# Optimization experiments

Measured on AMD Instinct MI355X. Metric: run time of the kernel, lower is better.

Reference implementation:

```python
import jax, jax.numpy as jnp
import numpy as np

D = 1024      # d_model
H = 16        # n_heads
KVH = 4       # num_kv_heads
DH = D // H   # head_dim = 64
CHUNK = 256
SDIM = 128
MG = 8        # m_global
B, T = 4, 4096


def setup_inputs() -> dict:
    key = jax.random.key(0)
    ks = jax.random.split(key, 12)
    s = 0.02
    mk = lambda i, shape: jax.random.normal(ks[i], shape, jnp.float32) * s
    return dict(
        x=jax.random.normal(ks[0], (B, T, D), jnp.float32),
        state=jnp.zeros((B, SDIM), jnp.float32),
        Wq=mk(1, (D, D)), Wk=mk(2, (KVH * DH, D)), Wv=mk(3, (KVH * DH, D)),
        Wo=mk(4, (D, D)), bo=jnp.zeros((D,), jnp.float32),
        ln_attn_g=jnp.ones((D,), jnp.float32), ln_attn_b=jnp.zeros((D,), jnp.float32),
        ln_ffn_g=jnp.ones((D,), jnp.float32), ln_ffn_b=jnp.zeros((D,), jnp.float32),
        W1=mk(5, (4 * D, D)), b1=jnp.zeros((4 * D,), jnp.float32),
        W2=mk(6, (D, 4 * D)), b2=jnp.zeros((D,), jnp.float32),
        Wsp=mk(7, (SDIM, D)), bsp=jnp.zeros((SDIM,), jnp.float32),
        Wsi=mk(8, (D, SDIM)), bsi=jnp.zeros((D,), jnp.float32),
        gtok=mk(9, (MG, D)),
    )


def _ln(x, g, b):
    m = x.mean(-1, keepdims=True)
    v = ((x - m) ** 2).mean(-1, keepdims=True)
    return (x - m) / jnp.sqrt(v + 1e-5) * g + b


def reference(x, state, Wq, Wk, Wv, Wo, bo, ln_attn_g, ln_attn_b,
              ln_ffn_g, ln_ffn_b, W1, b1, W2, b2, Wsp, bsp, Wsi, bsi, gtok):
    Bn, Tn, Dn = x.shape
    nchunks = Tn // CHUNK
    Tc = MG + CHUNK            # tokens per attention call (globals + chunk)
    G = H // KVH               # query heads per KV head
    causal = jnp.tril(jnp.ones((Tc, Tc), bool))
    scale = 1.0 / np.sqrt(DH).astype(np.float32)

    def step(st, chunk):  # st:[B,SDIM], chunk:[B,CHUNK,D]
        h = _ln(chunk, ln_attn_g, ln_attn_b) + (st @ Wsi.T + bsi)[:, None, :]
        h_in = jnp.concatenate([jnp.broadcast_to(gtok, (Bn, MG, Dn)), h], axis=1)
        q = (h_in @ Wq.T).reshape(Bn, Tc, H, DH)
        k = (h_in @ Wk.T).reshape(Bn, Tc, KVH, DH)
        v = (h_in @ Wv.T).reshape(Bn, Tc, KVH, DH)
        # GQA: group query heads over shared KV heads
        qg = q.reshape(Bn, Tc, KVH, G, DH)
        scores = jnp.einsum('bqhgd,bkhd->bhgqk', qg * scale, k)
        scores = jnp.where(causal, scores, -jnp.inf)
        attn = jax.nn.softmax(scores, axis=-1)
        o = jnp.einsum('bhgqk,bkhd->bqhgd', attn, v).reshape(Bn, Tc, Dn)
        y = (o @ Wo.T + bo)[:, MG:, :]
        c = chunk + y
        ff = jax.nn.gelu(_ln(c, ln_ffn_g, ln_ffn_b) @ W1.T + b1, approximate=False) @ W2.T + b2
        c = c + ff
        new_st = c.mean(axis=1) @ Wsp.T + bsp
        return new_st, c

    chunks = x.reshape(Bn, nchunks, CHUNK, Dn).transpose(1, 0, 2, 3)
    final_state, outs = jax.lax.scan(step, state, chunks)
    y_full = outs.transpose(1, 0, 2, 3).reshape(Bn, Tn, Dn)
    return y_full, final_state
```

## Files before the change

### kernel.cpp

```cpp
#include <hip/hip_runtime.h>
#include <hip/hip_bf16.h>

#define Dm    1024
#define Hn    16
#define KVH   4
#define DH    64
#define CHUNK 256
#define SDIM  128
#define MG    8
#define Bn    4
#define Tn    4096
#define TC    264
#define NSTEP 16
#define TD    4194304L

typedef __attribute__((ext_vector_type(8))) short short8;
typedef __attribute__((ext_vector_type(4))) float floatx4;
typedef __hip_bfloat16 bf16;

__device__ __forceinline__ void gl16(const void* g, void* l) {
    using GP = const __attribute__((address_space(1))) char*;
    using LP = __attribute__((address_space(3))) char*;
    __builtin_amdgcn_global_load_lds((GP)g, (LP)l, 16, 0, 0);
}
__device__ __forceinline__ float b2f(short s) {
    unsigned int u = ((unsigned int)(unsigned short)s) << 16;
    float f; __builtin_memcpy(&f, &u, 4); return f;
}
__device__ __forceinline__ short f2b(float f) {
    bf16 h = __float2bfloat16(f);
    short s; __builtin_memcpy(&s, &h, 2); return s;
}


__global__ __launch_bounds__(512) void vcopy_k(const float* __restrict__ s, float* __restrict__ d, int n) {
    int i = blockIdx.x * 512 + threadIdx.x;
    if (i < n) d[i] = s[i];
}

__global__ __launch_bounds__(256) void cvt_bf16_k(const float* __restrict__ s, bf16* __restrict__ d, int n4) {
    int i = blockIdx.x * 256 + threadIdx.x;
    if (i >= n4) return;
    float4 v = ((const float4*)s)[i];
    bf16* o = d + i * 4;
    o[0] = __float2bfloat16(v.x); o[1] = __float2bfloat16(v.y);
    o[2] = __float2bfloat16(v.z); o[3] = __float2bfloat16(v.w);
}

__global__ __launch_bounds__(256) void wsiT_k(const float* __restrict__ Wsi, bf16* __restrict__ WsiT) {
    int idx = blockIdx.x * 256 + threadIdx.x;
    int s = idx >> 10, d = idx & 1023;
    WsiT[idx] = __float2bfloat16(Wsi[d * SDIM + s]);
}

__global__ __launch_bounds__(64) void bfused_k(const bf16* __restrict__ wqkv, const float* __restrict__ bsi,
                                               float* __restrict__ bfused) {
    int n = blockIdx.x * 64 + threadIdx.x;
    const bf16* wr = wqkv + (long)n * 1024;
    float a = 0.f;
    for (int k8 = 0; k8 < 128; ++k8) {
        short8 wv = *(const short8*)(wr + k8 * 8);
#pragma unroll
        for (int e = 0; e < 8; ++e) a += b2f(wv[e]) * bsi[k8 * 8 + e];
    }
    bfused[n] = a;
}

__global__ __launch_bounds__(256) void lng_k(const float* __restrict__ x, const float* __restrict__ gtok,
                                             const float* __restrict__ g, const float* __restrict__ be,
                                             bf16* __restrict__ lnxg, int gstep) {
    int bx = blockIdx.x, b = blockIdx.y, tid = threadIdx.x;
    int sl = bx / 264, r = bx - sl * 264;
    bf16* orow = lnxg + (long)((sl * 4 + b) * 264 + r) * 1024 + tid * 4;
    if (r < MG) {
        float4 v = *(const float4*)(gtok + r * 1024 + tid * 4);
        orow[0] = __float2bfloat16(v.x); orow[1] = __float2bfloat16(v.y);
        orow[2] = __float2bfloat16(v.z); orow[3] = __float2bfloat16(v.w);
        return;
    }
    const float* row = x + (long)b * TD + ((long)(gstep * 4 + sl) * 256 + (r - MG)) * 1024;
    float4 v = *(const float4*)(row + tid * 4);
    float s = v.x + v.y + v.z + v.w;
    float q = v.x * v.x + v.y * v.y + v.z * v.z + v.w * v.w;
    for (int off = 32; off > 0; off >>= 1) { s += __shfl_down(s, off); q += __shfl_down(q, off); }
    __shared__ float red[10];
    int w = tid >> 6;
    if ((tid & 63) == 0) { red[w] = s; red[4 + w] = q; }
    __syncthreads();
    if (tid == 0) {
        float ts = red[0] + red[1] + red[2] + red[3];
        float tq = red[4] + red[5] + red[6] + red[7];
        float mean = ts * (1.f / Dm);
        float var = tq * (1.f / Dm) - mean * mean;
        red[8] = mean;
        red[9] = rsqrtf(var + 1e-5f);
    }
    __syncthreads();
    float mean = red[8], rstd = red[9];
    int d = tid * 4;
    float4 gv = *(const float4*)(g + d);
    float4 bv = *(const float4*)(be + d);
    orow[0] = __float2bfloat16((v.x - mean) * rstd * gv.x + bv.x);
    orow[1] = __float2bfloat16((v.y - mean) * rstd * gv.y + bv.y);
    orow[2] = __float2bfloat16((v.z - mean) * rstd * gv.z + bv.z);
    orow[3] = __float2bfloat16((v.w - mean) * rstd * gv.w + bv.w);
}

template<int BN>
__global__ __launch_bounds__(256) void gemm64(
    const bf16* __restrict__ A, const bf16* __restrict__ W,
    int M, int N, int K, int kspan,
    bf16* __restrict__ Cb, int ldc, const float* __restrict__ bias, int gelu,
    float* __restrict__ Cpart, long partMN)
{
    constexpr int NSEG = 4 + BN / 16;
    constexpr int SEGW = NSEG / 4;
    constexpr int FC   = BN / 64;
    constexpr int WN   = BN / 4;
    constexpr int HALFB = NSEG * 1024;
    constexpr int PHB   = 2 * HALFB;
    __shared__ short S[PHB];

    int tid = threadIdx.x;
    int w = tid >> 6, l = tid & 63;
    int m0 = blockIdx.y << 6, n0 = blockIdx.x * BN;
    long kb = (long)blockIdx.z * kspan;

    const bf16* gp[SEGW];
    int so[SEGW];
#pragma unroll
    for (int si = 0; si < SEGW; ++si) {
        int s = w + si * 4;
        const bf16* base = (s < 4) ? (A + (long)(m0 + s * 16 + (l >> 2)) * K)
                                   : (W + (long)(n0 + (s - 4) * 16 + (l >> 2)) * K);
        gp[si] = base + ((l & 3) << 3) + kb;
        so[si] = s * 1024 + l * 16;
    }
    char* cS = (char*)S;

    floatx4 acc[4][FC];
#pragma unroll
    for (int t = 0; t < 4; ++t)
#pragma unroll
        for (int u = 0; u < FC; ++u) acc[t][u] = (floatx4){0.f, 0.f, 0.f, 0.f};

    int arow = l & 15;
    int acol = (l >> 4) << 3;
    int np = kspan >> 6;

#define STAGE(p)                                                         \
    {                                                                    \
        int kt_ = (p) << 6;                                              \
        char* b_ = cS + ((p) & 1) * PHB;                                 \
        _Pragma("unroll")                                                \
        for (int si = 0; si < SEGW; ++si) {                              \
            gl16(gp[si] + kt_, b_ + so[si]);                             \
            gl16(gp[si] + kt_ + 32, b_ + HALFB + so[si]);                \
        }                                                                \
    }

    STAGE(0)
    for (int p = 0; p < np; ++p) {
        if (p + 1 < np) {
            STAGE(p + 1)
            if constexpr (SEGW == 2) asm volatile("s_waitcnt vmcnt(4)" ::: "memory");
            else                     asm volatile("s_waitcnt vmcnt(6)" ::: "memory");
        } else {
            asm volatile("s_waitcnt vmcnt(0)" ::: "memory");
        }
        __builtin_amdgcn_s_barrier();
        __builtin_amdgcn_sched_barrier(0);
        const short* buf = S + (p & 1) * (PHB / 2);
#pragma unroll
        for (int kh = 0; kh < 2; ++kh) {
            const short* hb = buf + kh * (HALFB / 2);
            short8 a[4], b[FC];
#pragma unroll
            for (int t = 0; t < 4; ++t)
                a[t] = *(const short8*)&hb[(t * 16 + arow) * 32 + acol];
#pragma unroll
            for (int u = 0; u < FC; ++u)
                b[u] = *(const short8*)&hb[2048 + (w * WN + u * 16 + arow) * 32 + acol];
#pragma unroll
            for (int t = 0; t < 4; ++t)
#pragma unroll
                for (int u = 0; u < FC; ++u)
                    acc[t][u] = __builtin_amdgcn_mfma_f32_16x16x32_bf16(a[t], b[u], acc[t][u], 0, 0, 0);
        }
        __builtin_amdgcn_sched_barrier(0);
        __builtin_amdgcn_s_barrier();
    }
#undef STAGE

    int crow0 = m0 + ((l >> 4) << 2);
    int ccol0 = n0 + w * WN + (l & 15);
    if (Cpart) {
        float* pp = Cpart + (long)blockIdx.z * partMN;
#pragma unroll
        for (int t = 0; t < 4; ++t)
#pragma unroll
            for (int rr = 0; rr < 4; ++rr) {
                int m = crow0 + t * 16 + rr;
                if (m >= M) continue;
#pragma unroll
                for (int u = 0; u < FC; ++u)
                    pp[(long)m * N + ccol0 + u * 16] = acc[t][u][rr];
            }
    } else {
#pragma unroll
        for (int t = 0; t < 4; ++t)
#pragma unroll
            for (int rr = 0; rr < 4; ++rr) {
                int m = crow0 + t * 16 + rr;
                if (m >= M) continue;
                bf16* crow = Cb + (long)m * ldc;
#pragma unroll
                for (int u = 0; u < FC; ++u) {
                    int n = ccol0 + u * 16;
                    float v = acc[t][u][rr];
                    if (bias) v += bias[n];
                    if (gelu) v = 0.5f * v * (1.f + erff(v * 0.70710678118654752f));
                    crow[n] = __float2bfloat16(v);
                }
            }
    }
}

__global__ __launch_bounds__(256) void reduce_ln_k(const float* __restrict__ part,
                                                   const float* __restrict__ bo,
                                                   const float* __restrict__ x,
                                                   float* __restrict__ out, long roff,
                                                   const float* __restrict__ g,
                                                   const float* __restrict__ be,
                                                   bf16* __restrict__ t_ln) {
    int m = blockIdx.x;
    int b = m >> 8, r = m & 255;
    int tid = threadIdx.x;
    long ro = (long)b * TD + (roff + r) * 1024L + tid * 4;
    int pi = m * 256 + tid;
    float4 s  = ((const float4*)part)[pi];
    float4 p2 = ((const float4*)(part + 1048576))[pi];
    float4 bv = ((const float4*)bo)[tid];
    float4 rv = *(const float4*)(x + ro);
    float c0 = s.x + p2.x + bv.x + rv.x;
    float c1 = s.y + p2.y + bv.y + rv.y;
    float c2 = s.z + p2.z + bv.z + rv.z;
    float c3 = s.w + p2.w + bv.w + rv.w;
    *(float4*)(out + ro) = make_float4(c0, c1, c2, c3);
    float sum = c0 + c1 + c2 + c3;
    float sq  = c0 * c0 + c1 * c1 + c2 * c2 + c3 * c3;
    for (int off = 32; off > 0; off >>= 1) { sum += __shfl_down(sum, off); sq += __shfl_down(sq, off); }
    __shared__ float red[10];
    int w = tid >> 6;
    if ((tid & 63) == 0) { red[w] = sum; red[4 + w] = sq; }
    __syncthreads();
    if (tid == 0) {
        float ts = red[0] + red[1] + red[2] + red[3];
        float tq = red[4] + red[5] + red[6] + red[7];
        float mean = ts * (1.f / Dm);
        float var = tq * (1.f / Dm) - mean * mean;
        red[8] = mean;
        red[9] = rsqrtf(var + 1e-5f);
    }
    __syncthreads();
    float mean = red[8], rstd = red[9];
    float4 gv = ((const float4*)g)[tid];
    float4 bev = ((const float4*)be)[tid];
    bf16* orow = t_ln + (long)(b * CHUNK + r) * Dm + tid * 4;
    orow[0] = __float2bfloat16((c0 - mean) * rstd * gv.x + bev.x);
    orow[1] = __float2bfloat16((c1 - mean) * rstd * gv.y + bev.y);
    orow[2] = __float2bfloat16((c2 - mean) * rstd * gv.z + bev.z);
    orow[3] = __float2bfloat16((c3 - mean) * rstd * gv.w + bev.w);
}

__global__ __launch_bounds__(256) void reduce_colpart_k(const float* __restrict__ part,
                                                        const float* __restrict__ bias,
                                                        float* __restrict__ out, long roff,
                                                        float* __restrict__ colp) {
    int b = blockIdx.x, rg = blockIdx.y, tid = threadIdx.x;
    float4 bv = ((const float4*)bias)[tid];
    float4 cs = make_float4(0.f, 0.f, 0.f, 0.f);
#pragma unroll
    for (int r8 = 0; r8 < 8; ++r8) {
        int r = rg * 8 + r8;
        int pi = (b * 256 + r) * 256 + tid;
        float4 s  = ((const float4*)part)[pi];
        float4 p2 = ((const float4*)(part + 1048576))[pi];
        long ro = (long)b * TD + (roff + r) * 1024L + tid * 4;
        float4 rv = *(const float4*)(out + ro);
        float4 v = make_float4(s.x + p2.x + bv.x + rv.x, s.y + p2.y + bv.y + rv.y,
                               s.z + p2.z + bv.z + rv.z, s.w + p2.w + bv.w + rv.w);
        *(float4*)(out + ro) = v;
        cs.x += v.x; cs.y += v.y; cs.z += v.z; cs.w += v.w;
    }
    *(float4*)(colp + ((b * 32 + rg) << 10) + tid * 4) = cs;
}

__global__ __launch_bounds__(256) void state_update_k(const float* __restrict__ colp,
                                                      const float* __restrict__ Wsp,
                                                      const float* __restrict__ bsp,
                                                      float* __restrict__ st) {
    int b = blockIdx.x;
    int tid = threadIdx.x, w = tid >> 6, l = tid & 63;
    int ss = blockIdx.y * 4 + w;
    float4 m[4];
#pragma unroll
    for (int t = 0; t < 4; ++t) m[t] = make_float4(0.f, 0.f, 0.f, 0.f);
    for (int rg = 0; rg < 32; ++rg) {
        const float* pr = colp + ((b * 32 + rg) << 10) + l * 16;
#pragma unroll
        for (int t = 0; t < 4; ++t) {
            float4 v = *(const float4*)(pr + t * 4);
            m[t].x += v.x; m[t].y += v.y; m[t].z += v.z; m[t].w += v.w;
        }
    }
    const float* wr = Wsp + (long)ss * Dm + l * 16;
    float a = 0.f;
#pragma unroll
    for (int t = 0; t < 4; ++t) {
        float4 wv = *(const float4*)(wr + t * 4);
        a += m[t].x * wv.x + m[t].y * wv.y + m[t].z * wv.z + m[t].w * wv.w;
    }
    a *= (1.f / CHUNK);
    for (int off = 32; off > 0; off >>= 1) a += __shfl_down(a, off);
    if (l == 0) st[b * SDIM + ss] = a + bsp[ss];
}

__global__ __launch_bounds__(256) void attn_mfma_k(const bf16* __restrict__ qkv,
                                                   const float* __restrict__ st,
                                                   const bf16* __restrict__ Wf,
                                                   const float* __restrict__ bfused,
                                                   bf16* __restrict__ o_mat) {
    int qc = blockIdx.x, head = blockIdx.y, b = blockIdx.z;
    int kvh = head >> 2;
    int tid = threadIdx.x, w = tid >> 6, l = tid & 63;
    int m16 = l & 15, h4 = l >> 4;

    __shared__ short Qs[64][64];
    __shared__ short Ks[64][64];
    __shared__ short Vt[64][64];
    __shared__ short Ps[4][16][64];
    __shared__ float sq[64], sk[64], sv[64];

    const long rowq0 = (long)b * TC + MG + qc * 64;
    const bf16* kbase = qkv + ((long)b * TC) * 1536 + 1024 + kvh * DH;
    const bf16* vbase = kbase + 256;

    if (tid < 192) {
        int which = tid >> 6, nn = tid & 63;
        int n = (which == 0) ? head * 64 + nn
              : (which == 1) ? 1024 + kvh * 64 + nn
                             : 1280 + kvh * 64 + nn;
        const bf16* wr = Wf + (long)n * SDIM;
        const float* sr = st + b * SDIM;
        float a = bfused[n];
#pragma unroll
        for (int k8 = 0; k8 < 16; ++k8) {
            short8 wv = *(const short8*)(wr + k8 * 8);
#pragma unroll
            for (int e = 0; e < 8; ++e) a += sr[k8 * 8 + e] * b2f(wv[e]);
        }
        if (which == 0) sq[nn] = a; else if (which == 1) sk[nn] = a; else sv[nn] = a;
    }
    __syncthreads();

#pragma unroll
    for (int p = 0; p < 2; ++p) {
        int rr = p * 32 + (tid >> 3);
        int c0 = (tid & 7) * 8;
        short8 v = *(const short8*)(qkv + (rowq0 + rr) * 1536 + head * DH + c0);
        short8 o;
#pragma unroll
        for (int e = 0; e < 8; ++e) o[e] = f2b(b2f(v[e]) + sq[c0 + e]);
        *(short8*)&Qs[rr][c0] = o;
    }

    float a_m[4] = {-1e30f, -1e30f, -1e30f, -1e30f};
    float a_l[4] = {0.f, 0.f, 0.f, 0.f};
    floatx4 acc_o[4];
#pragma unroll
    for (int dt = 0; dt < 4; ++dt) acc_o[dt] = (floatx4){0.f, 0.f, 0.f, 0.f};
    short8 aq[2];

    int qtok0 = MG + qc * 64 + w * 16 + h4 * 4;
    int ntiles = qc + 2;

    for (int t = 0; t < ntiles; ++t) {
        int jt = t * 64;
#pragma unroll
        for (int p = 0; p < 2; ++p) {
            int rr = p * 32 + (tid >> 3);
            int c0 = (tid & 7) * 8;
            int gk = min(jt + rr, TC - 1);
            short8 v = *(const short8*)(kbase + (long)gk * 1536 + c0);
            short8 o;
            if (gk >= MG) {
#pragma unroll
                for (int e = 0; e < 8; ++e) o[e] = f2b(b2f(v[e]) + sk[c0 + e]);
            } else o = v;
            *(short8*)&Ks[rr][c0] = o;
        }
#pragma unroll
        for (int p = 0; p < 2; ++p) {
            int cg = p * 4 + w;
            int gk = min(jt + l, TC - 1);
            short8 vv = *(const short8*)(vbase + (long)gk * 1536 + cg * 8);
            if (gk >= MG) {
#pragma unroll
                for (int e = 0; e < 8; ++e) vv[e] = f2b(b2f(vv[e]) + sv[cg * 8 + e]);
            }
#pragma unroll
            for (int e = 0; e < 8; ++e) Vt[cg * 8 + e][l] = vv[e];
        }
        __syncthreads();
        if (t == 0) {
            aq[0] = *(const short8*)&Qs[w * 16 + m16][h4 * 8];
            aq[1] = *(const short8*)&Qs[w * 16 + m16][32 + h4 * 8];
        }
        floatx4 s[4];
#pragma unroll
        for (int st_ = 0; st_ < 4; ++st_) {
            s[st_] = (floatx4){0.f, 0.f, 0.f, 0.f};
#pragma unroll
            for (int c = 0; c < 2; ++c) {
                short8 kf = *(const short8*)&Ks[st_ * 16 + m16][c * 32 + h4 * 8];
                s[st_] = __builtin_amdgcn_mfma_f32_16x16x32_bf16(aq[c], kf, s[st_], 0, 0, 0);
            }
        }
#pragma unroll
        for (int st_ = 0; st_ < 4; ++st_) {
            int keyg = jt + st_ * 16 + m16;
#pragma unroll
            for (int r = 0; r < 4; ++r) {
                float v = s[st_][r] * 0.125f;
                s[st_][r] = (keyg > qtok0 + r) ? -1e30f : v;
            }
        }
#pragma unroll
        for (int r = 0; r < 4; ++r) {
            float tm = fmaxf(fmaxf(s[0][r], s[1][r]), fmaxf(s[2][r], s[3][r]));
            tm = fmaxf(tm, __shfl_xor(tm, 1));
            tm = fmaxf(tm, __shfl_xor(tm, 2));
            tm = fmaxf(tm, __shfl_xor(tm, 4));
            tm = fmaxf(tm, __shfl_xor(tm, 8));
            float mn = fmaxf(a_m[r], tm);
            float rs = __expf(a_m[r] - mn);
            a_m[r] = mn;
            float ps = 0.f;
#pragma unroll
            for (int st_ = 0; st_ < 4; ++st_) {
                float p = __expf(s[st_][r] - mn);
                s[st_][r] = p;
                ps += p;
            }
            ps += __shfl_xor(ps, 1); ps += __shfl_xor(ps, 2);
            ps += __shfl_xor(ps, 4); ps += __shfl_xor(ps, 8);
            a_l[r] = a_l[r] * rs + ps;
#pragma unroll
            for (int dt = 0; dt < 4; ++dt) acc_o[dt][r] *= rs;
#pragma unroll
            for (int st_ = 0; st_ < 4; ++st_) {
                Ps[w][h4 * 4 + r][st_ * 16 + m16] = f2b(s[st_][r]);
            }
        }
#pragma unroll
        for (int c = 0; c < 2; ++c) {
            short8 ap = *(const short8*)&Ps[w][m16][c * 32 + h4 * 8];
#pragma unroll
            for (int dt = 0; dt < 4; ++dt) {
                short8 vf = *(const short8*)&Vt[dt * 16 + m16][c * 32 + h4 * 8];
                acc_o[dt] = __builtin_amdgcn_mfma_f32_16x16x32_bf16(ap, vf, acc_o[dt], 0, 0, 0);
            }
        }
        __syncthreads();
    }

#pragma unroll
    for (int r = 0; r < 4; ++r) {
        float inv = 1.f / a_l[r];
        long row = (long)b * CHUNK + qc * 64 + w * 16 + h4 * 4 + r;
#pragma unroll
        for (int dt = 0; dt < 4; ++dt)
            o_mat[row * Dm + head * DH + dt * 16 + m16] = __float2bfloat16(acc_o[dt][r] * inv);
    }
}


extern "C" void kernel_launch(void* const* d_in, const int* in_sizes, int n_in,
                              void* d_out, int out_size, void* d_ws, size_t ws_size,
                              hipStream_t stream) {
    const float* x     = (const float*)d_in[0];
    const float* state = (const float*)d_in[1];
    const float* Wq    = (const float*)d_in[2];
    const float* Wk    = (const float*)d_in[3];
    const float* Wv    = (const float*)d_in[4];
    const float* Wo    = (const float*)d_in[5];
    const float* bo    = (const float*)d_in[6];
    const float* lag   = (const float*)d_in[7];
    const float* lab   = (const float*)d_in[8];
    const float* lfg   = (const float*)d_in[9];
    const float* lfb   = (const float*)d_in[10];
    const float* W1    = (const float*)d_in[11];
    const float* b1    = (const float*)d_in[12];
    const float* W2    = (const float*)d_in[13];
    const float* b2    = (const float*)d_in[14];
    const float* Wsp   = (const float*)d_in[15];
    const float* bsp   = (const float*)d_in[16];
    const float* Wsi   = (const float*)d_in[17];
    const float* bsi   = (const float*)d_in[18];
    const float* gtok  = (const float*)d_in[19];

    float* out = (float*)d_out;
    char*  wsb = (char*)d_ws;

    bf16* wqkv   = (bf16*)(wsb);
    bf16* wo     = (bf16*)(wsb + 3145728);
    bf16* w1     = (bf16*)(wsb + 5242880);
    bf16* w2     = (bf16*)(wsb + 13631488);
    bf16* Wfused = (bf16*)(wsb + 22020096);
    bf16* WsiT   = (bf16*)(wsb + 22413312);
    float* bfused= (float*)(wsb + 22675456);
    float* st    = (float*)(wsb + 22706176);
    bf16* qkvg   = (bf16*)(wsb + 22708224);
    char* R1     = wsb + 35684352;
    bf16* lnxg   = (bf16*)R1;
    bf16* u      = (bf16*)R1;
    float* part  = (float*)(wsb + 44335104);
    char* scrB   = wsb + 52723712;
    bf16* o_mat  = (bf16*)scrB;
    bf16* t_ln   = (bf16*)scrB;
    float* colp  = (float*)scrB;

    vcopy_k<<<1, 512, 0, stream>>>(state, st, 512);
    cvt_bf16_k<<<1024, 256, 0, stream>>>(Wq, wqkv,            262144);
    cvt_bf16_k<<< 256, 256, 0, stream>>>(Wk, wqkv + 1048576,   65536);
    cvt_bf16_k<<< 256, 256, 0, stream>>>(Wv, wqkv + 1310720,   65536);
    cvt_bf16_k<<<1024, 256, 0, stream>>>(Wo, wo,              262144);
    cvt_bf16_k<<<4096, 256, 0, stream>>>(W1, w1,             1048576);
    cvt_bf16_k<<<4096, 256, 0, stream>>>(W2, w2,             1048576);
    wsiT_k<<<512, 256, 0, stream>>>(Wsi, WsiT);
    gemm64<64><<<dim3(2, 24, 1), 256, 0, stream>>>(
        wqkv, WsiT, 1536, 128, 1024, 1024,
        Wfused, 128, nullptr, 0, nullptr, 0L);
    bfused_k<<<24, 64, 0, stream>>>(wqkv, bsi, bfused);

    for (int s = 0; s < NSTEP; ++s) {
        long roff = (long)s * CHUNK;
        if ((s & 3) == 0) {
            int g = s >> 2;
            lng_k<<<dim3(1056, 4), 256, 0, stream>>>(x, gtok, lag, lab, lnxg, g);
            gemm64<128><<<dim3(12, 66, 1), 256, 0, stream>>>(
                lnxg, wqkv, 4224, 1536, 1024, 1024,
                qkvg, 1536, nullptr, 0, nullptr, 0L);
        }
        const bf16* qkv_s = qkvg + (long)(s & 3) * (4 * 264 * 1536);
        attn_mfma_k<<<dim3(4, 16, 4), 256, 0, stream>>>(qkv_s, st, Wfused, bfused, o_mat);
        gemm64<64><<<dim3(16, 16, 2), 256, 0, stream>>>(
            o_mat, wo, Bn * CHUNK, 1024, 1024, 512,
            nullptr, 0, nullptr, 0, part, 1048576L);
        reduce_ln_k<<<1024, 256, 0, stream>>>(part, bo, x, out, roff, lfg, lfb, t_ln);
        gemm64<128><<<dim3(32, 16, 1), 256, 0, stream>>>(
            t_ln, w1, Bn * CHUNK, 4096, 1024, 1024,
            u, 4096, b1, 1, nullptr, 0L);
        gemm64<64><<<dim3(16, 16, 2), 256, 0, stream>>>(
            u, w2, Bn * CHUNK, 1024, 4096, 2048,
            nullptr, 0, nullptr, 0, part, 1048576L);
        reduce_colpart_k<<<dim3(4, 32), 256, 0, stream>>>(part, b2, out, roff, colp);
        state_update_k<<<dim3(4, 32), 256, 0, stream>>>(colp, Wsp, bsp, st);
    }
    vcopy_k<<<1, 512, 0, stream>>>(st, out + (long)Bn * Tn * Dm, 512);
}
```

Measured before the change: 1.540 ms.

## Prefetch next K/V tile into registers and widen W2 split-K to four

The attention kernel now loads the next K/V tile into registers right after the barrier, so global load latency overlaps with the current tile's MFMA work. The W2 GEMM uses four K-splits when the workspace is large enough, giving more blocks to fill the GPU, and the reduction kernel now sums a variable number of partials. The cost is more registers in attention, extra partial-buffer traffic, and scratch placement that depends on workspace size.

```diff
diff --git a/kernel.cpp b/kernel.cpp
--- a/kernel.cpp
+++ b/kernel.cpp
@@ -273,7 +273,7 @@
     orow[3] = __float2bfloat16((c3 - mean) * rstd * gv.w + bev.w);
 }
 
-__global__ __launch_bounds__(256) void reduce_colpart_k(const float* __restrict__ part,
+__global__ __launch_bounds__(256) void reduce_colpart_k(const float* __restrict__ part, int KS,
                                                         const float* __restrict__ bias,
                                                         float* __restrict__ out, long roff,
                                                         float* __restrict__ colp) {
@@ -284,12 +284,15 @@
     for (int r8 = 0; r8 < 8; ++r8) {
         int r = rg * 8 + r8;
         int pi = (b * 256 + r) * 256 + tid;
-        float4 s  = ((const float4*)part)[pi];
-        float4 p2 = ((const float4*)(part + 1048576))[pi];
+        float4 s = ((const float4*)part)[pi];
+        for (int z = 1; z < KS; ++z) {
+            float4 p = ((const float4*)(part + (long)z * 1048576))[pi];
+            s.x += p.x; s.y += p.y; s.z += p.z; s.w += p.w;
+        }
         long ro = (long)b * TD + (roff + r) * 1024L + tid * 4;
         float4 rv = *(const float4*)(out + ro);
-        float4 v = make_float4(s.x + p2.x + bv.x + rv.x, s.y + p2.y + bv.y + rv.y,
-                               s.z + p2.z + bv.z + rv.z, s.w + p2.w + bv.w + rv.w);
+        float4 v = make_float4(s.x + bv.x + rv.x, s.y + bv.y + rv.y,
+                               s.z + bv.z + rv.z, s.w + bv.w + rv.w);
         *(float4*)(out + ro) = v;
         cs.x += v.x; cs.y += v.y; cs.z += v.z; cs.w += v.w;
     }
@@ -384,27 +387,45 @@
 
     int qtok0 = MG + qc * 64 + w * 16 + h4 * 4;
     int ntiles = qc + 2;
-
+    int ck0 = (tid & 7) * 8;
+
+    short8 kreg[2], vreg[2];
+#define LOADKV(TT)                                                          \
+    {                                                                       \
+        int jt_ = (TT) * 64;                                                \
+        _Pragma("unroll")                                                   \
+        for (int p = 0; p < 2; ++p) {                                       \
+            int rr = p * 32 + (tid >> 3);                                   \
+            int gk = min(jt_ + rr, TC - 1);                                 \
+            kreg[p] = *(const short8*)(kbase + (long)gk * 1536 + ck0);      \
+        }                                                                   \
+        _Pragma("unroll")                                                   \
+        for (int p = 0; p < 2; ++p) {                                       \
+            int cg = p * 4 + w;                                             \
+            int gk = min(jt_ + l, TC - 1);                                  \
+            vreg[p] = *(const short8*)(vbase + (long)gk * 1536 + cg * 8);   \
+        }                                                                   \
+    }
+
+    LOADKV(0)
     for (int t = 0; t < ntiles; ++t) {
         int jt = t * 64;
 #pragma unroll
         for (int p = 0; p < 2; ++p) {
             int rr = p * 32 + (tid >> 3);
-            int c0 = (tid & 7) * 8;
             int gk = min(jt + rr, TC - 1);
-            short8 v = *(const short8*)(kbase + (long)gk * 1536 + c0);
-            short8 o;
+            short8 o = kreg[p];
             if (gk >= MG) {
 #pragma unroll
-                for (int e = 0; e < 8; ++e) o[e] = f2b(b2f(v[e]) + sk[c0 + e]);
-            } else o = v;
-            *(short8*)&Ks[rr][c0] = o;
+                for (int e = 0; e < 8; ++e) o[e] = f2b(b2f(o[e]) + sk[ck0 + e]);
+            }
+            *(short8*)&Ks[rr][ck0] = o;
         }
 #pragma unroll
         for (int p = 0; p < 2; ++p) {
             int cg = p * 4 + w;
             int gk = min(jt + l, TC - 1);
-            short8 vv = *(const short8*)(vbase + (long)gk * 1536 + cg * 8);
+            short8 vv = vreg[p];
             if (gk >= MG) {
 #pragma unroll
                 for (int e = 0; e < 8; ++e) vv[e] = f2b(b2f(vv[e]) + sv[cg * 8 + e]);
@@ -413,6 +434,7 @@
             for (int e = 0; e < 8; ++e) Vt[cg * 8 + e][l] = vv[e];
         }
         __syncthreads();
+        if (t + 1 < ntiles) LOADKV(t + 1)
         if (t == 0) {
             aq[0] = *(const short8*)&Qs[w * 16 + m16][h4 * 8];
             aq[1] = *(const short8*)&Qs[w * 16 + m16][32 + h4 * 8];
@@ -474,6 +496,7 @@
         }
         __syncthreads();
     }
+#undef LOADKV
 
 #pragma unroll
     for (int r = 0; r < 4; ++r) {
@@ -513,6 +536,8 @@
     float* out = (float*)d_out;
     char*  wsb = (char*)d_ws;
 
+    const int ksF = (ws_size >= (size_t)63300000) ? 4 : 2;
+
     bf16* wqkv   = (bf16*)(wsb);
     bf16* wo     = (bf16*)(wsb + 3145728);
     bf16* w1     = (bf16*)(wsb + 5242880);
@@ -526,7 +551,7 @@
     bf16* lnxg   = (bf16*)R1;
     bf16* u      = (bf16*)R1;
     float* part  = (float*)(wsb + 44335104);
-    char* scrB   = wsb + 52723712;
+    char* scrB   = wsb + 44335104 + (size_t)ksF * 4194304;
     bf16* o_mat  = (bf16*)scrB;
     bf16* t_ln   = (bf16*)scrB;
     float* colp  = (float*)scrB;
@@ -562,10 +587,10 @@
         gemm64<128><<<dim3(32, 16, 1), 256, 0, stream>>>(
             t_ln, w1, Bn * CHUNK, 4096, 1024, 1024,
             u, 4096, b1, 1, nullptr, 0L);
-        gemm64<64><<<dim3(16, 16, 2), 256, 0, stream>>>(
-            u, w2, Bn * CHUNK, 1024, 4096, 2048,
+        gemm64<64><<<dim3(16, 16, ksF), 256, 0, stream>>>(
+            u, w2, Bn * CHUNK, 1024, 4096, 4096 / ksF,
             nullptr, 0, nullptr, 0, part, 1048576L);
-        reduce_colpart_k<<<dim3(4, 32), 256, 0, stream>>>(part, b2, out, roff, colp);
+        reduce_colpart_k<<<dim3(4, 32), 256, 0, stream>>>(part, ksF, b2, out, roff, colp);
         state_update_k<<<dim3(4, 32), 256, 0, stream>>>(colp, Wsp, bsp, st);
     }
     vcopy_k<<<1, 512, 0, stream>>>(st, out + (long)Bn * Tn * Dm, 512);
```

Result: slower. 1.609 ms (+4.5%).
